# Performance work log

Hardware: AMD Instinct MI355X
Metric: run time of the kernel (lower is better)

The kernel has to match this reference:

```python
import jax, jax.numpy as jnp
import numpy as np
from jax import lax

NUM_HEADS = 4
FIN = 4096
FOUT = 4096


def setup_inputs() -> dict:
    key = jax.random.key(0)
    k1, k2, k3, k4, k5 = jax.random.split(key, 5)
    inp = jax.random.normal(k1, (2, 2048, FIN), dtype=jnp.float32)
    # xavier-uniform-like scale for the fc weight
    lim = float(np.sqrt(6.0 / (FIN + FOUT)))
    W = jax.random.uniform(k2, (FOUT, FIN), minval=-lim, maxval=lim, dtype=jnp.float32)
    # per-head 3x3 conv kernels (Conv2d(1, 1, 3, 3) per head, stacked OIHW)
    conv_w = jax.random.normal(k3, (NUM_HEADS, 1, 3, 3), dtype=jnp.float32) * (1.0 / 3.0)
    conv_b = jax.random.normal(k4, (NUM_HEADS,), dtype=jnp.float32) * 0.1
    sk_wt = jax.random.normal(k5, (NUM_HEADS, 1, 1), dtype=jnp.float32)
    return {"inp": inp, "W": W, "conv_w": conv_w, "conv_b": conv_b, "sk_wt": sk_wt}


def _transform_weight(W, conv_w, conv_b, sk_wt):
    # W: [fout, fin] -> [num_heads, fout/num_heads, fin]
    mat = W.reshape(NUM_HEADS, FOUT // NUM_HEADS, FIN)
    # per-head 3x3 conv == grouped conv with feature_group_count = num_heads
    x = mat[None]  # [1, H=num_heads, fout/h, fin]
    y = lax.conv_general_dilated(
        x, conv_w,
        window_strides=(1, 1),
        padding=((1, 1), (1, 1)),
        feature_group_count=NUM_HEADS,
        dimension_numbers=("NCHW", "OIHW", "NCHW"),
    )[0] + conv_b[:, None, None]
    # sigmoid-gated residual: out + sigmoid(sk_wt) * mat
    out = y + jax.nn.sigmoid(sk_wt) * mat
    return out.reshape(FOUT, FIN)


def reference(inp, W, conv_w, conv_b, sk_wt):
    W_i = _transform_weight(W, conv_w, conv_b, sk_wt)
    # F.linear(inp, W_i) with bias=None
    return jnp.einsum("bsf,of->bso", inp, W_i)
```

## Files before the change

kernel.cpp:

```cpp
#include <hip/hip_runtime.h>
#include <hip/hip_bf16.h>

#define FIN 4096
#define FOUT 4096
#define HEADS 4
#define ROWS_PER_HEAD (FOUT / HEADS)
#define M_DIM 4096

typedef __attribute__((ext_vector_type(8))) short bf16x8;
typedef __attribute__((ext_vector_type(4))) float floatx4;

__global__ __launch_bounds__(256) void cast_to_bf16(
    const float* __restrict__ x, __hip_bfloat16* __restrict__ y) {
  int idx = blockIdx.x * 256 + threadIdx.x;
  const float4* xv = (const float4*)x;
  float4 a = xv[idx * 2];
  float4 b = xv[idx * 2 + 1];
  __hip_bfloat16 t[8];
  t[0] = __float2bfloat16(a.x); t[1] = __float2bfloat16(a.y);
  t[2] = __float2bfloat16(a.z); t[3] = __float2bfloat16(a.w);
  t[4] = __float2bfloat16(b.x); t[5] = __float2bfloat16(b.y);
  t[6] = __float2bfloat16(b.z); t[7] = __float2bfloat16(b.w);
  *(bf16x8*)(&y[(size_t)idx * 8]) = *(bf16x8*)t;
}

__global__ __launch_bounds__(256) void transform_w(
    const float* __restrict__ W,
    const float* __restrict__ cw,
    const float* __restrict__ cb,
    const float* __restrict__ sk,
    __hip_bfloat16* __restrict__ Wt) {
  int gid = blockIdx.x * 256 + threadIdx.x;
  int o = gid >> 9;
  int fs = (gid & 511) << 3;
  int h = o >> 10;
  int r = o & (ROWS_PER_HEAD - 1);

  float kk[3][3];
#pragma unroll
  for (int i = 0; i < 3; i++)
#pragma unroll
    for (int j = 0; j < 3; j++) kk[i][j] = cw[h * 9 + i * 3 + j];
  float sig = 1.0f / (1.0f + __expf(-sk[h]));

  float acc[8];
#pragma unroll
  for (int j = 0; j < 8; j++) acc[j] = cb[h];

#pragma unroll
  for (int dr = -1; dr <= 1; dr++) {
    int rr = r + dr;
    if (rr < 0 || rr >= ROWS_PER_HEAD) continue;
    const float* rp = W + ((size_t)(h * ROWS_PER_HEAD + rr)) * FIN + fs;
    float a[10];
    float4 v0 = *(const float4*)rp;
    float4 v1 = *(const float4*)(rp + 4);
    a[1] = v0.x; a[2] = v0.y; a[3] = v0.z; a[4] = v0.w;
    a[5] = v1.x; a[6] = v1.y; a[7] = v1.z; a[8] = v1.w;
    a[0] = (fs > 0) ? rp[-1] : 0.0f;
    a[9] = (fs + 8 < FIN) ? rp[8] : 0.0f;
#pragma unroll
    for (int j = 0; j < 8; j++)
      acc[j] += kk[dr + 1][0] * a[j] + kk[dr + 1][1] * a[j + 1] +
                kk[dr + 1][2] * a[j + 2];
    if (dr == 0) {
#pragma unroll
      for (int j = 0; j < 8; j++) acc[j] += sig * a[j + 1];
    }
  }
  __hip_bfloat16 t[8];
#pragma unroll
  for (int j = 0; j < 8; j++) t[j] = __float2bfloat16(acc[j]);
  *(bf16x8*)(&Wt[(size_t)o * FIN + fs]) = *(bf16x8*)t;
}

__device__ static inline void gload_lds16(const __hip_bfloat16* g,
                                          __hip_bfloat16* l) {
  __builtin_amdgcn_global_load_lds(
      (const __attribute__((address_space(1))) void*)g,
      (__attribute__((address_space(3))) void*)l, 16, 0, 0);
}

__global__ __launch_bounds__(256, 3) void gemm_nt(
    const __hip_bfloat16* __restrict__ A,
    const __hip_bfloat16* __restrict__ B,
    float* __restrict__ C,
    int M, int N, int K) {
  __shared__ __hip_bfloat16 As[128 * 32];
  __shared__ __hip_bfloat16 Bs[128 * 32];

  const int tid = threadIdx.x;
  const int lane = tid & 63;
  const int wave = tid >> 6;
  const int tile_m = blockIdx.y * 128;
  const int tile_n = blockIdx.x * 128;

  const int fr = lane & 15;
  const int quad = lane >> 4;
  const int wm = (wave & 1) * 64;
  const int wn = (wave >> 1) * 64;
  const int sel = (fr >> 1) & 3;
  const int koff = (quad ^ sel) * 8;

  floatx4 acc[4][4];
#pragma unroll
  for (int i = 0; i < 4; i++)
#pragma unroll
    for (int j = 0; j < 4; j++) acc[i][j] = (floatx4){0.f, 0.f, 0.f, 0.f};

  for (int k0 = 0; k0 < K; k0 += 32) {
#pragma unroll
    for (int t = 0; t < 2; t++) {
      int base_chunk = (t * 4 + wave) * 64;
      int p = base_chunk + lane;
      int row = p >> 2;
      int kq = ((p & 3) ^ ((row >> 1) & 3)) * 8;
      gload_lds16(&A[(size_t)(tile_m + row) * K + k0 + kq],
                  &As[base_chunk * 8]);
      gload_lds16(&B[(size_t)(tile_n + row) * K + k0 + kq],
                  &Bs[base_chunk * 8]);
    }
    __syncthreads();

    bf16x8 a_frag[4], b_frag[4];
#pragma unroll
    for (int i = 0; i < 4; i++) {
      a_frag[i] = *(const bf16x8*)(&As[(wm + i * 16 + fr) * 32 + koff]);
      b_frag[i] = *(const bf16x8*)(&Bs[(wn + i * 16 + fr) * 32 + koff]);
    }
#pragma unroll
    for (int i = 0; i < 4; i++)
#pragma unroll
      for (int j = 0; j < 4; j++)
        acc[i][j] = __builtin_amdgcn_mfma_f32_16x16x32_bf16(
            a_frag[i], b_frag[j], acc[i][j], 0, 0, 0);
    __syncthreads();
  }

#pragma unroll
  for (int i = 0; i < 4; i++) {
    int m_base = tile_m + wm + i * 16 + quad * 4;
#pragma unroll
    for (int j = 0; j < 4; j++) {
      int n = tile_n + wn + j * 16 + fr;
#pragma unroll
      for (int r = 0; r < 4; r++) {
        C[(size_t)(m_base + r) * N + n] = acc[i][j][r];
      }
    }
  }
}

extern "C" void kernel_launch(void* const* d_in, const int* in_sizes, int n_in,
                              void* d_out, int out_size, void* d_ws,
                              size_t ws_size, hipStream_t stream) {
  const float* inp = (const float*)d_in[0];
  const float* W = (const float*)d_in[1];
  const float* conv_w = (const float*)d_in[2];
  const float* conv_b = (const float*)d_in[3];
  const float* sk_wt = (const float*)d_in[4];
  float* out = (float*)d_out;

  __hip_bfloat16* Wt = (__hip_bfloat16*)d_ws;
  __hip_bfloat16* Ab =
      (__hip_bfloat16*)((char*)d_ws + (size_t)(32u << 20));

  cast_to_bf16<<<(M_DIM * FIN) / (256 * 8), 256, 0, stream>>>(inp, Ab);
  transform_w<<<(FOUT * FIN / 8) / 256, 256, 0, stream>>>(W, conv_w, conv_b,
                                                          sk_wt, Wt);
  dim3 grid(FOUT / 128, M_DIM / 128);
  gemm_nt<<<grid, 256, 0, stream>>>(Ab, Wt, out, M_DIM, FOUT, FIN);
}
```

Measured before the change: 326.7 us.

## Fuse fp32-to-bf16 input cast into GEMM via fp32 LDS staging

```diff
diff --git a/kernel.cpp b/kernel.cpp
--- a/kernel.cpp
+++ b/kernel.cpp
@@ -9,20 +9,6 @@
 
 typedef __attribute__((ext_vector_type(8))) short bf16x8;
 typedef __attribute__((ext_vector_type(4))) float floatx4;
-
-__global__ __launch_bounds__(256) void cast_to_bf16(
-    const float* __restrict__ x, __hip_bfloat16* __restrict__ y) {
-  int idx = blockIdx.x * 256 + threadIdx.x;
-  const float4* xv = (const float4*)x;
-  float4 a = xv[idx * 2];
-  float4 b = xv[idx * 2 + 1];
-  __hip_bfloat16 t[8];
-  t[0] = __float2bfloat16(a.x); t[1] = __float2bfloat16(a.y);
-  t[2] = __float2bfloat16(a.z); t[3] = __float2bfloat16(a.w);
-  t[4] = __float2bfloat16(b.x); t[5] = __float2bfloat16(b.y);
-  t[6] = __float2bfloat16(b.z); t[7] = __float2bfloat16(b.w);
-  *(bf16x8*)(&y[(size_t)idx * 8]) = *(bf16x8*)t;
-}
 
 __global__ __launch_bounds__(256) void transform_w(
     const float* __restrict__ W,
@@ -74,19 +60,18 @@
   *(bf16x8*)(&Wt[(size_t)o * FIN + fs]) = *(bf16x8*)t;
 }
 
-__device__ static inline void gload_lds16(const __hip_bfloat16* g,
-                                          __hip_bfloat16* l) {
+__device__ static inline void gload_lds16(const void* g, void* l) {
   __builtin_amdgcn_global_load_lds(
       (const __attribute__((address_space(1))) void*)g,
       (__attribute__((address_space(3))) void*)l, 16, 0, 0);
 }
 
 __global__ __launch_bounds__(256, 3) void gemm_nt(
-    const __hip_bfloat16* __restrict__ A,
+    const float* __restrict__ A,
     const __hip_bfloat16* __restrict__ B,
     float* __restrict__ C,
     int M, int N, int K) {
-  __shared__ __hip_bfloat16 As[128 * 32];
+  __shared__ float As[128 * 32];
   __shared__ __hip_bfloat16 Bs[128 * 32];
 
   const int tid = threadIdx.x;
@@ -99,8 +84,11 @@
   const int quad = lane >> 4;
   const int wm = (wave & 1) * 64;
   const int wn = (wave >> 1) * 64;
-  const int sel = (fr >> 1) & 3;
-  const int koff = (quad ^ sel) * 8;
+
+  const int koffB = (quad ^ ((fr >> 1) & 3)) * 8;
+  const int selA = fr & 7;
+  const int sA0 = (2 * quad) ^ selA;
+  const int sA1 = (2 * quad + 1) ^ selA;
 
   floatx4 acc[4][4];
 #pragma unroll
@@ -110,23 +98,39 @@
 
   for (int k0 = 0; k0 < K; k0 += 32) {
 #pragma unroll
+    for (int t = 0; t < 4; t++) {
+      int base = (t * 4 + wave) * 64;
+      int p = base + lane;
+      int row = p >> 3;
+      int g = (p & 7) ^ (row & 7);
+      gload_lds16(&A[(size_t)(tile_m + row) * K + k0 + g * 4],
+                  &As[base * 4]);
+    }
+#pragma unroll
     for (int t = 0; t < 2; t++) {
-      int base_chunk = (t * 4 + wave) * 64;
-      int p = base_chunk + lane;
+      int base = (t * 4 + wave) * 64;
+      int p = base + lane;
       int row = p >> 2;
       int kq = ((p & 3) ^ ((row >> 1) & 3)) * 8;
-      gload_lds16(&A[(size_t)(tile_m + row) * K + k0 + kq],
-                  &As[base_chunk * 8]);
       gload_lds16(&B[(size_t)(tile_n + row) * K + k0 + kq],
-                  &Bs[base_chunk * 8]);
+                  &Bs[base * 8]);
     }
     __syncthreads();
 
     bf16x8 a_frag[4], b_frag[4];
 #pragma unroll
     for (int i = 0; i < 4; i++) {
-      a_frag[i] = *(const bf16x8*)(&As[(wm + i * 16 + fr) * 32 + koff]);
-      b_frag[i] = *(const bf16x8*)(&Bs[(wn + i * 16 + fr) * 32 + koff]);
+      const float* ap = &As[(wm + i * 16 + fr) * 32];
+      floatx4 lo = *(const floatx4*)(ap + sA0 * 4);
+      floatx4 hi = *(const floatx4*)(ap + sA1 * 4);
+      __hip_bfloat16 t8[8];
+#pragma unroll
+      for (int j = 0; j < 4; j++) {
+        t8[j] = __float2bfloat16(lo[j]);
+        t8[4 + j] = __float2bfloat16(hi[j]);
+      }
+      a_frag[i] = *(bf16x8*)t8;
+      b_frag[i] = *(const bf16x8*)(&Bs[(wn + i * 16 + fr) * 32 + koffB]);
     }
 #pragma unroll
     for (int i = 0; i < 4; i++)
@@ -162,12 +166,9 @@
   float* out = (float*)d_out;
 
   __hip_bfloat16* Wt = (__hip_bfloat16*)d_ws;
-  __hip_bfloat16* Ab =
-      (__hip_bfloat16*)((char*)d_ws + (size_t)(32u << 20));
 
-  cast_to_bf16<<<(M_DIM * FIN) / (256 * 8), 256, 0, stream>>>(inp, Ab);
   transform_w<<<(FOUT * FIN / 8) / 256, 256, 0, stream>>>(W, conv_w, conv_b,
                                                           sk_wt, Wt);
   dim3 grid(FOUT / 128, M_DIM / 128);
-  gemm_nt<<<grid, 256, 0, stream>>>(Ab, Wt, out, M_DIM, FOUT, FIN);
+  gemm_nt<<<grid, 256, 0, stream>>>(inp, Wt, out, M_DIM, FOUT, FIN);
 }
```

Measured after the change: 383.2 us. 1.17x slower.
